# Kernel tuning notes

Measured on AMD Instinct MI355X. Metric: run time of the kernel, lower is better.

Reference implementation:

```python
import jax, jax.numpy as jnp
import numpy as np

N_NODES = 100000
N_EDGES = 1200000
F_IN, F_HID, F_OUT = 128, 64, 40


def gcn_conv(x, W, b, src, dst, n):
    # PyG GCNConv: h = x @ W; add self-loops; symmetric norm; scatter-add; + bias
    h = x @ W  # [N, F]
    loops = jnp.arange(n)
    s = jnp.concatenate([src, loops])
    d = jnp.concatenate([dst, loops])
    deg = jnp.zeros((n,), x.dtype).at[d].add(jnp.asarray(1.0, x.dtype))
    dis = jax.lax.rsqrt(deg)  # deg >= 1 thanks to self-loops
    norm = dis[s] * dis[d]  # [E+N]
    msg = h[s] * norm[:, None]  # gather + scale
    out = jnp.zeros((n, h.shape[1]), x.dtype).at[d].add(msg)  # scatter-add
    return out + b


def setup_inputs() -> dict:
    key = jax.random.key(0)
    ks = jax.random.split(key, 8)
    sc = lambda f: 1.0 / np.sqrt(f)
    return {
        "x": jax.random.normal(ks[0], (N_NODES, F_IN), jnp.float32),
        "edge_index": jax.random.randint(ks[1], (2, N_EDGES), 0, N_NODES, jnp.int64),
        "W1": jax.random.normal(ks[2], (F_IN, F_HID), jnp.float32) * sc(F_IN),
        "b1": jnp.zeros((F_HID,), jnp.float32),
        "W2": jax.random.normal(ks[3], (F_HID, F_HID), jnp.float32) * sc(F_HID),
        "b2": jnp.zeros((F_HID,), jnp.float32),
        "W3": jax.random.normal(ks[4], (F_HID, F_OUT), jnp.float32) * sc(F_HID),
        "b3": jnp.zeros((F_OUT,), jnp.float32),
    }


def reference(x, edge_index, W1, b1, W2, b2, W3, b3):
    src, dst = edge_index[0], edge_index[1]
    n = x.shape[0]
    h = jax.nn.relu(gcn_conv(x, W1, b1, src, dst, n))  # dropout is identity (eval)
    h = jax.nn.relu(gcn_conv(h, W2, b2, src, dst, n))
    out = gcn_conv(h, W3, b3, src, dst, n)
    return jax.nn.log_softmax(out, axis=1)
```

## Files before the change

kernel.cpp:

```cpp
#include <hip/hip_runtime.h>
#include <math.h>


static inline int cdiv(long a, int b) { return (int)((a + b - 1) / b); }

__device__ __forceinline__ unsigned short f2bf(float f) {
    unsigned u = __float_as_uint(f);
    u += 0x7fffu + ((u >> 16) & 1u);
    return (unsigned short)(u >> 16);
}
__device__ __forceinline__ float bf2f(unsigned short b) {
    return __uint_as_float(((unsigned)b) << 16);
}

#define RSH 9
#define RNODES 512
#define GB 256
#define NBMAX 256

__global__ __launch_bounds__(256)
void k_bhist(const int* __restrict__ dst, int* __restrict__ bh,
             int E, int NB, int EPB) {
    __shared__ int bcnt[NBMAX];
    const int tid = threadIdx.x, blk = blockIdx.x;
    for (int i = tid; i < NB; i += 256) bcnt[i] = 0;
    __syncthreads();
    const int e1 = min(E, (blk + 1) * EPB);
    for (int e = blk * EPB + tid; e < e1; e += 256)
        atomicAdd(&bcnt[dst[e] >> RSH], 1);
    __syncthreads();
    for (int i = tid; i < NB; i += 256) bh[i * GB + blk] = bcnt[i];
}

__global__ __launch_bounds__(256)
void k_bscatter(const int* __restrict__ src, const int* __restrict__ dst,
                const int* __restrict__ eoff, int2* __restrict__ ebuf,
                int E, int NB, int EPB) {
    __shared__ int cur[NBMAX];
    const int tid = threadIdx.x, blk = blockIdx.x;
    for (int i = tid; i < NB; i += 256) cur[i] = eoff[i * GB + blk];
    __syncthreads();
    const int e1 = min(E, (blk + 1) * EPB);
    for (int e = blk * EPB + tid; e < e1; e += 256) {
        int d = dst[e];
        int s = src[e];
        int pos = atomicAdd(&cur[d >> RSH], 1);
        ebuf[pos] = make_int2(d, s);
    }
}

__global__ __launch_bounds__(1024)
void k_csr(const int2* __restrict__ ebuf, const int* __restrict__ eoff,
           int* __restrict__ rp, float* __restrict__ dis, int* __restrict__ esrc,
           int N, int E, int NB) {
    __shared__ int cnt[RNODES];
    __shared__ int cur[RNODES];
    __shared__ int sm[1024];
    const int tid = threadIdx.x, b = blockIdx.x;
    const int node0 = b << RSH;
    const int bb = eoff[b * GB];
    const int be = (b + 1 == NB) ? E : eoff[(b + 1) * GB];

    if (tid < RNODES) cnt[tid] = 0;
    __syncthreads();
    for (int e = bb + tid; e < be; e += 1024)
        atomicAdd(&cnt[ebuf[e].x - node0], 1);
    __syncthreads();

    int v = (tid < RNODES) ? cnt[tid] : 0;
    sm[tid] = v;
    __syncthreads();
    for (int off = 1; off < RNODES; off <<= 1) {
        int t = (tid >= off) ? sm[tid - off] : 0;
        __syncthreads();
        sm[tid] += t;
        __syncthreads();
    }
    if (tid < RNODES) {
        int excl = sm[tid] - v;
        cur[tid] = excl;
        int node = node0 + tid;
        if (node < N) {
            rp[node] = bb + excl;
            dis[node] = rsqrtf(1.0f + (float)v);
        }
    }
    if (b == 0 && tid == 0) rp[N] = E;
    __syncthreads();

    for (int e = bb + tid; e < be; e += 1024) {
        int2 ev = ebuf[e];
        int slot = atomicAdd(&cur[ev.x - node0], 1);
        esrc[bb + slot] = ev.y;
    }
}

#define SCAN_B 1024
__global__ void k_scan1(const int* __restrict__ cnt, int* __restrict__ rp,
                        int* __restrict__ bsum, int n) {
    __shared__ int sm[SCAN_B];
    const int tid = threadIdx.x;
    const int gid = blockIdx.x * SCAN_B + tid;
    int v = (gid < n) ? cnt[gid] : 0;
    sm[tid] = v;
    __syncthreads();
    for (int off = 1; off < SCAN_B; off <<= 1) {
        int t = (tid >= off) ? sm[tid - off] : 0;
        __syncthreads();
        sm[tid] += t;
        __syncthreads();
    }
    if (gid < n) rp[gid] = sm[tid] - v;
    if (tid == SCAN_B - 1) bsum[blockIdx.x] = sm[tid];
}

__global__ void k_scan2(int* __restrict__ bsum, int nb) {
    __shared__ int sm[SCAN_B];
    const int tid = threadIdx.x;
    int v = (tid < nb) ? bsum[tid] : 0;
    sm[tid] = v;
    __syncthreads();
    for (int off = 1; off < SCAN_B; off <<= 1) {
        int t = (tid >= off) ? sm[tid - off] : 0;
        __syncthreads();
        sm[tid] += t;
        __syncthreads();
    }
    if (tid < nb) bsum[tid] = sm[tid] - v;
}

__global__ void k_scan3(int* __restrict__ rp, const int* __restrict__ bsum, int n, int E) {
    const int gid = blockIdx.x * SCAN_B + threadIdx.x;
    if (gid < n) rp[gid] += bsum[gid / SCAN_B];
    if (gid == n) rp[n] = E;
}

__device__ __forceinline__ void fma4(float a, const float4& w, float4& acc) {
    acc.x = fmaf(a, w.x, acc.x);
    acc.y = fmaf(a, w.y, acc.y);
    acc.z = fmaf(a, w.z, acc.z);
    acc.w = fmaf(a, w.w, acc.w);
}

template<int K, bool BF16OUT>
__global__ __launch_bounds__(256, 2)
void k_gemm_lds(const float* __restrict__ X, const float* __restrict__ W,
                const float* __restrict__ dis, void* __restrict__ Hout, int N) {
    constexpr int KP = K + 4;
    __shared__ float xs[64 * KP];
    __shared__ float wsh[K * 64];
    const int tid = threadIdx.x;
    const int tx = tid & 15;
    const int ty = tid >> 4;
    const int row0 = blockIdx.x * 64;

    {
        const float4* Wg = (const float4*)W;
        float4* Wl = (float4*)wsh;
#pragma unroll
        for (int i = 0; i < K * 16 / 256; ++i)
            Wl[i * 256 + tid] = Wg[i * 256 + tid];
    }
    {
        constexpr int F4 = K / 4;
        for (int i = tid; i < 64 * F4; i += 256) {
            int r = i / F4, c = i - r * F4;
            int gr = min(row0 + r, N - 1);
            float4 v = *(const float4*)(X + (size_t)gr * K + c * 4);
            *(float4*)(xs + r * KP + c * 4) = v;
        }
    }
    __syncthreads();

    float4 acc0 = {0.f, 0.f, 0.f, 0.f};
    float4 acc1 = {0.f, 0.f, 0.f, 0.f};
    float4 acc2 = {0.f, 0.f, 0.f, 0.f};
    float4 acc3 = {0.f, 0.f, 0.f, 0.f};

    const float* xr0 = xs + (ty * 4 + 0) * KP;
    const float* xr1 = xs + (ty * 4 + 1) * KP;
    const float* xr2 = xs + (ty * 4 + 2) * KP;
    const float* xr3 = xs + (ty * 4 + 3) * KP;

#pragma unroll 2
    for (int k = 0; k < K; k += 4) {
        float4 w0 = *(const float4*)(wsh + (k + 0) * 64 + tx * 4);
        float4 w1 = *(const float4*)(wsh + (k + 1) * 64 + tx * 4);
        float4 w2 = *(const float4*)(wsh + (k + 2) * 64 + tx * 4);
        float4 w3 = *(const float4*)(wsh + (k + 3) * 64 + tx * 4);
        float4 xa = *(const float4*)(xr0 + k);
        float4 xb = *(const float4*)(xr1 + k);
        float4 xc = *(const float4*)(xr2 + k);
        float4 xd = *(const float4*)(xr3 + k);

        fma4(xa.x, w0, acc0); fma4(xa.y, w1, acc0); fma4(xa.z, w2, acc0); fma4(xa.w, w3, acc0);
        fma4(xb.x, w0, acc1); fma4(xb.y, w1, acc1); fma4(xb.z, w2, acc1); fma4(xb.w, w3, acc1);
        fma4(xc.x, w0, acc2); fma4(xc.y, w1, acc2); fma4(xc.z, w2, acc2); fma4(xc.w, w3, acc2);
        fma4(xd.x, w0, acc3); fma4(xd.y, w1, acc3); fma4(xd.z, w2, acc3); fma4(xd.w, w3, acc3);
    }

    const int r = row0 + ty * 4;
#pragma unroll
    for (int i = 0; i < 4; ++i) {
        if (r + i >= N) break;
        float4 a = (i == 0) ? acc0 : (i == 1) ? acc1 : (i == 2) ? acc2 : acc3;
        float d = dis[r + i];
        a.x *= d; a.y *= d; a.z *= d; a.w *= d;
        if (BF16OUT) {
            ushort4 o;
            o.x = f2bf(a.x); o.y = f2bf(a.y); o.z = f2bf(a.z); o.w = f2bf(a.w);
            *(ushort4*)((unsigned short*)Hout + (size_t)(r + i) * 64 + tx * 4) = o;
        } else {
            *(float4*)((float*)Hout + (size_t)(r + i) * 64 + tx * 4) = a;
        }
    }
}

template<int MODE>
__global__ __launch_bounds__(256, 8)
void k_agg(const unsigned short* __restrict__ Hs, const float* __restrict__ dis,
           const int* __restrict__ rp, const int* __restrict__ esrc,
           const float* __restrict__ bias, void* __restrict__ A, int N) {
    const int wave = threadIdx.x >> 6;
    const int lane = threadIdx.x & 63;
    const int node = blockIdx.x * (blockDim.x >> 6) + wave;
    if (node >= N) return;
    const int q  = lane >> 4;
    const int f4 = lane & 15;

    const int e0 = rp[node];
    const int e1 = rp[node + 1];
    float4 acc = {0.f, 0.f, 0.f, 0.f};
    int e = e0 + q;
    for (; e + 4 < e1; e += 8) {
        int s0 = esrc[e];
        int s1 = esrc[e + 4];
        ushort4 h0 = *(const ushort4*)(Hs + (size_t)s0 * 64 + f4 * 4);
        ushort4 h1 = *(const ushort4*)(Hs + (size_t)s1 * 64 + f4 * 4);
        acc.x += bf2f(h0.x) + bf2f(h1.x);
        acc.y += bf2f(h0.y) + bf2f(h1.y);
        acc.z += bf2f(h0.z) + bf2f(h1.z);
        acc.w += bf2f(h0.w) + bf2f(h1.w);
    }
    for (; e < e1; e += 4) {
        int s = esrc[e];
        ushort4 h = *(const ushort4*)(Hs + (size_t)s * 64 + f4 * 4);
        acc.x += bf2f(h.x); acc.y += bf2f(h.y); acc.z += bf2f(h.z); acc.w += bf2f(h.w);
    }
    acc.x += __shfl_xor(acc.x, 16, 64);
    acc.y += __shfl_xor(acc.y, 16, 64);
    acc.z += __shfl_xor(acc.z, 16, 64);
    acc.w += __shfl_xor(acc.w, 16, 64);
    acc.x += __shfl_xor(acc.x, 32, 64);
    acc.y += __shfl_xor(acc.y, 32, 64);
    acc.z += __shfl_xor(acc.z, 32, 64);
    acc.w += __shfl_xor(acc.w, 32, 64);

    if (lane < 16) {
        const float dd = dis[node];
        ushort4 sh = *(const ushort4*)(Hs + (size_t)node * 64 + lane * 4);
        float4 v;
        v.x = (acc.x + bf2f(sh.x)) * dd;
        v.y = (acc.y + bf2f(sh.y)) * dd;
        v.z = (acc.z + bf2f(sh.z)) * dd;
        v.w = (acc.w + bf2f(sh.w)) * dd;
        if (MODE == 0 || MODE == 1) {
            float4 bv = ((const float4*)bias)[lane];
            v.x = fmaxf(v.x + bv.x, 0.f);
            v.y = fmaxf(v.y + bv.y, 0.f);
            v.z = fmaxf(v.z + bv.z, 0.f);
            v.w = fmaxf(v.w + bv.w, 0.f);
        }
        if (MODE == 1) {
            v.x *= dd; v.y *= dd; v.z *= dd; v.w *= dd;
            ushort4 o;
            o.x = f2bf(v.x); o.y = f2bf(v.y); o.z = f2bf(v.z); o.w = f2bf(v.w);
            *(ushort4*)((unsigned short*)A + (size_t)node * 64 + lane * 4) = o;
        } else {
            *(float4*)((float*)A + (size_t)node * 64 + lane * 4) = v;
        }
    }
}

__global__ __launch_bounds__(256, 4)
void k_w3lsm(const float* __restrict__ X, const float* __restrict__ W,
             const float* __restrict__ bias, float* __restrict__ out,
             int N, int npw) {
    const int wid  = blockIdx.x * (blockDim.x >> 6) + (threadIdx.x >> 6);
    const int lane = threadIdx.x & 63;
    const int cl   = (lane < 40) ? lane : 0;

    float w[64];
#pragma unroll
    for (int k = 0; k < 64; ++k) w[k] = W[k * 40 + cl];
    const float bv = bias[cl];

    const int n0 = wid * npw;
    const int n1 = min(n0 + npw, N);
    for (int node = n0; node < n1; ++node) {
        const int un = __builtin_amdgcn_readfirstlane(node);
        const float4* xr = (const float4*)(X + (size_t)un * 64);
        float acc = 0.0f;
#pragma unroll
        for (int j = 0; j < 16; ++j) {
            float4 xv = xr[j];
            acc = fmaf(xv.x, w[4 * j + 0], acc);
            acc = fmaf(xv.y, w[4 * j + 1], acc);
            acc = fmaf(xv.z, w[4 * j + 2], acc);
            acc = fmaf(xv.w, w[4 * j + 3], acc);
        }
        float v = (lane < 40) ? acc + bv : -INFINITY;
        float m = v;
#pragma unroll
        for (int o = 32; o > 0; o >>= 1) m = fmaxf(m, __shfl_xor(m, o, 64));
        float ex = (lane < 40) ? expf(v - m) : 0.0f;
        float s = ex;
#pragma unroll
        for (int o = 32; o > 0; o >>= 1) s += __shfl_xor(s, o, 64);
        if (lane < 40) out[(size_t)node * 40 + lane] = v - m - logf(s);
    }
}

extern "C" void kernel_launch(void* const* d_in, const int* in_sizes, int n_in,
                              void* d_out, int out_size, void* d_ws, size_t ws_size,
                              hipStream_t stream) {
    const float* x  = (const float*)d_in[0];
    const int*   ei = (const int*)d_in[1];
    const float* W1 = (const float*)d_in[2];
    const float* b1 = (const float*)d_in[3];
    const float* W2 = (const float*)d_in[4];
    const float* b2 = (const float*)d_in[5];
    const float* W3 = (const float*)d_in[6];
    const float* b3 = (const float*)d_in[7];
    float* out = (float*)d_out;

    const int N = in_sizes[0] / 128;
    const int E = in_sizes[1] / 2;
    const int* src = ei;
    const int* dst = ei + E;

    const int NB   = cdiv(N, RNODES);
    const int EPB  = cdiv(E, GB);
    const int nscan = NB * GB;

    char* ws = (char*)d_ws;
    char* buf0  = ws;                         ws += (size_t)N * 64 * sizeof(float);
    char* buf1  = ws;                         ws += (size_t)N * 64 * sizeof(float);
    int*   esrc  = (int*)ws;                  ws += (size_t)E * sizeof(int);
    int*   rp    = (int*)ws;                  ws += (size_t)(N + 1) * sizeof(int);
    int*   bsum  = (int*)ws;                  ws += (size_t)SCAN_B * sizeof(int);
    float* dis   = (float*)ws;                ws += (size_t)N * sizeof(float);
    int*   bh    = (int*)ws;                  ws += (size_t)nscan * sizeof(int);
    int*   eoff  = (int*)ws;                  ws += (size_t)(nscan + 1) * sizeof(int);
    int2*  ebuf  = (int2*)buf0;

    const int B = 256;
    const int nbs = cdiv(nscan, SCAN_B);

    k_bhist<<<GB, B, 0, stream>>>(dst, bh, E, NB, EPB);
    k_scan1<<<nbs, SCAN_B, 0, stream>>>(bh, eoff, bsum, nscan);
    k_scan2<<<1, SCAN_B, 0, stream>>>(bsum, nbs);
    k_scan3<<<cdiv(nscan + 1, SCAN_B), SCAN_B, 0, stream>>>(eoff, bsum, nscan, E);
    k_bscatter<<<GB, B, 0, stream>>>(src, dst, eoff, ebuf, E, NB, EPB);
    k_csr<<<NB, 1024, 0, stream>>>(ebuf, eoff, rp, dis, esrc, N, E, NB);

    k_gemm_lds<128, true><<<cdiv(N, 64), B, 0, stream>>>(x, W1, dis, buf0, N);
    k_agg<0><<<cdiv(N, 4), B, 0, stream>>>((const unsigned short*)buf0, dis, rp, esrc, b1, buf1, N);

    k_gemm_lds<64, true><<<cdiv(N, 64), B, 0, stream>>>((const float*)buf1, W2, dis, buf0, N);
    k_agg<1><<<cdiv(N, 4), B, 0, stream>>>((const unsigned short*)buf0, dis, rp, esrc, b2, buf1, N);

    k_agg<2><<<cdiv(N, 4), B, 0, stream>>>((const unsigned short*)buf1, dis, rp, esrc, nullptr, buf0, N);
    const int NW = 4096;
    const int npw = cdiv(N, NW);
    k_w3lsm<<<NW / 4, B, 0, stream>>>((const float*)buf0, W3, b3, out, N, npw);
}
```

Baseline: 336.7 us.

## Reorder layer 3 to transform before aggregating and fuse log_softmax into aggregation

Layer 3 now applies W3 first, producing a 40-wide bf16 Z from the pre-scaled 64-wide layer-2 output, and then aggregates over neighbours. This shrinks per-edge gather traffic from 64 to 40 features. The log_softmax is fused into the new aggregation kernel, which splits each node's edges across six lane groups of ten and reduces them through LDS. The k_agg bias/relu path was also made unconditional, but only modes 0 and 1 are still launched. The trade-off is an extra bf16 rounding of Z and 60 of 64 lanes active during the gather.

```diff
diff --git a/kernel.cpp b/kernel.cpp
--- a/kernel.cpp
+++ b/kernel.cpp
@@ -264,13 +264,11 @@
         v.y = (acc.y + bf2f(sh.y)) * dd;
         v.z = (acc.z + bf2f(sh.z)) * dd;
         v.w = (acc.w + bf2f(sh.w)) * dd;
-        if (MODE == 0 || MODE == 1) {
-            float4 bv = ((const float4*)bias)[lane];
-            v.x = fmaxf(v.x + bv.x, 0.f);
-            v.y = fmaxf(v.y + bv.y, 0.f);
-            v.z = fmaxf(v.z + bv.z, 0.f);
-            v.w = fmaxf(v.w + bv.w, 0.f);
-        }
+        float4 bv = ((const float4*)bias)[lane];
+        v.x = fmaxf(v.x + bv.x, 0.f);
+        v.y = fmaxf(v.y + bv.y, 0.f);
+        v.z = fmaxf(v.z + bv.z, 0.f);
+        v.w = fmaxf(v.w + bv.w, 0.f);
         if (MODE == 1) {
             v.x *= dd; v.y *= dd; v.z *= dd; v.w *= dd;
             ushort4 o;
@@ -283,9 +281,8 @@
 }
 
 __global__ __launch_bounds__(256, 4)
-void k_w3lsm(const float* __restrict__ X, const float* __restrict__ W,
-             const float* __restrict__ bias, float* __restrict__ out,
-             int N, int npw) {
+void k_zgemm(const unsigned short* __restrict__ A2s, const float* __restrict__ W,
+             unsigned short* __restrict__ Z, int N, int npw) {
     const int wid  = blockIdx.x * (blockDim.x >> 6) + (threadIdx.x >> 6);
     const int lane = threadIdx.x & 63;
     const int cl   = (lane < 40) ? lane : 0;
@@ -293,31 +290,94 @@
     float w[64];
 #pragma unroll
     for (int k = 0; k < 64; ++k) w[k] = W[k * 40 + cl];
-    const float bv = bias[cl];
 
     const int n0 = wid * npw;
     const int n1 = min(n0 + npw, N);
     for (int node = n0; node < n1; ++node) {
         const int un = __builtin_amdgcn_readfirstlane(node);
-        const float4* xr = (const float4*)(X + (size_t)un * 64);
+        const uint4* xr = (const uint4*)(A2s + (size_t)un * 64);
         float acc = 0.0f;
 #pragma unroll
-        for (int j = 0; j < 16; ++j) {
-            float4 xv = xr[j];
-            acc = fmaf(xv.x, w[4 * j + 0], acc);
-            acc = fmaf(xv.y, w[4 * j + 1], acc);
-            acc = fmaf(xv.z, w[4 * j + 2], acc);
-            acc = fmaf(xv.w, w[4 * j + 3], acc);
-        }
-        float v = (lane < 40) ? acc + bv : -INFINITY;
-        float m = v;
-#pragma unroll
-        for (int o = 32; o > 0; o >>= 1) m = fmaxf(m, __shfl_xor(m, o, 64));
-        float ex = (lane < 40) ? expf(v - m) : 0.0f;
-        float s = ex;
-#pragma unroll
-        for (int o = 32; o > 0; o >>= 1) s += __shfl_xor(s, o, 64);
-        if (lane < 40) out[(size_t)node * 40 + lane] = v - m - logf(s);
+        for (int j = 0; j < 8; ++j) {
+            uint4 u = xr[j];
+            acc = fmaf(__uint_as_float(u.x << 16),          w[8 * j + 0], acc);
+            acc = fmaf(__uint_as_float(u.x & 0xffff0000u),  w[8 * j + 1], acc);
+            acc = fmaf(__uint_as_float(u.y << 16),          w[8 * j + 2], acc);
+            acc = fmaf(__uint_as_float(u.y & 0xffff0000u),  w[8 * j + 3], acc);
+            acc = fmaf(__uint_as_float(u.z << 16),          w[8 * j + 4], acc);
+            acc = fmaf(__uint_as_float(u.z & 0xffff0000u),  w[8 * j + 5], acc);
+            acc = fmaf(__uint_as_float(u.w << 16),          w[8 * j + 6], acc);
+            acc = fmaf(__uint_as_float(u.w & 0xffff0000u),  w[8 * j + 7], acc);
+        }
+        if (lane < 40) Z[(size_t)node * 40 + lane] = f2bf(acc);
+    }
+}
+
+__global__ __launch_bounds__(256, 8)
+void k_agg40lsm(const unsigned short* __restrict__ Z, const float* __restrict__ dis,
+                const int* __restrict__ rp, const int* __restrict__ esrc,
+                const float* __restrict__ b3, float* __restrict__ out, int N) {
+    __shared__ float4 red[4][64];
+    const int wave = threadIdx.x >> 6;
+    const int lane = threadIdx.x & 63;
+    int node = blockIdx.x * 4 + wave;
+    if (node >= N) node = N - 1;
+    const int q = lane / 10;
+    const int f = lane - q * 10;
+    const bool act = (q < 6);
+
+    const int e0 = rp[node];
+    const int e1 = rp[node + 1];
+    float4 acc = {0.f, 0.f, 0.f, 0.f};
+    if (act) {
+        for (int e = e0 + q; e < e1; e += 6) {
+            int s = esrc[e];
+            ushort4 h = *(const ushort4*)(Z + (size_t)s * 40 + f * 4);
+            acc.x += bf2f(h.x); acc.y += bf2f(h.y); acc.z += bf2f(h.z); acc.w += bf2f(h.w);
+        }
+    }
+    red[wave][lane] = acc;
+    __syncthreads();
+
+    float4 v;
+    float m4 = -INFINITY;
+    if (lane < 10) {
+        float4 a0 = red[wave][lane];
+        float4 a1 = red[wave][10 + lane];
+        float4 a2 = red[wave][20 + lane];
+        float4 a3 = red[wave][30 + lane];
+        float4 a4 = red[wave][40 + lane];
+        float4 a5 = red[wave][50 + lane];
+        v.x = a0.x + a1.x + a2.x + a3.x + a4.x + a5.x;
+        v.y = a0.y + a1.y + a2.y + a3.y + a4.y + a5.y;
+        v.z = a0.z + a1.z + a2.z + a3.z + a4.z + a5.z;
+        v.w = a0.w + a1.w + a2.w + a3.w + a4.w + a5.w;
+        ushort4 sh = *(const ushort4*)(Z + (size_t)node * 40 + lane * 4);
+        const float dd = dis[node];
+        float4 bv = ((const float4*)b3)[lane];
+        v.x = (v.x + bf2f(sh.x)) * dd + bv.x;
+        v.y = (v.y + bf2f(sh.y)) * dd + bv.y;
+        v.z = (v.z + bf2f(sh.z)) * dd + bv.z;
+        v.w = (v.w + bf2f(sh.w)) * dd + bv.w;
+        m4 = fmaxf(fmaxf(v.x, v.y), fmaxf(v.z, v.w));
+    }
+    float m = m4;
+#pragma unroll
+    for (int o = 1; o < 16; o <<= 1) m = fmaxf(m, __shfl_xor(m, o, 64));
+    float es = 0.f;
+    if (lane < 10) {
+        es = expf(v.x - m) + expf(v.y - m) + expf(v.z - m) + expf(v.w - m);
+    }
+#pragma unroll
+    for (int o = 1; o < 16; o <<= 1) es += __shfl_xor(es, o, 64);
+    if (lane < 10) {
+        float ls = logf(es);
+        float4 o4;
+        o4.x = v.x - m - ls;
+        o4.y = v.y - m - ls;
+        o4.z = v.z - m - ls;
+        o4.w = v.w - m - ls;
+        *(float4*)(out + (size_t)node * 40 + lane * 4) = o4;
     }
 }
 
@@ -370,8 +430,10 @@
     k_gemm_lds<64, true><<<cdiv(N, 64), B, 0, stream>>>((const float*)buf1, W2, dis, buf0, N);
     k_agg<1><<<cdiv(N, 4), B, 0, stream>>>((const unsigned short*)buf0, dis, rp, esrc, b2, buf1, N);
 
-    k_agg<2><<<cdiv(N, 4), B, 0, stream>>>((const unsigned short*)buf1, dis, rp, esrc, nullptr, buf0, N);
-    const int NW = 4096;
+    const int NW = 8192;
     const int npw = cdiv(N, NW);
-    k_w3lsm<<<NW / 4, B, 0, stream>>>((const float*)buf0, W3, b3, out, N, npw);
-}
+    k_zgemm<<<NW / 4, B, 0, stream>>>((const unsigned short*)buf1, W3,
+                                      (unsigned short*)buf0, N, npw);
+    k_agg40lsm<<<cdiv(N, 4), B, 0, stream>>>((const unsigned short*)buf0, dis, rp, esrc,
+                                             b3, out, N);
+}
```

New measurement: 343.3 us. Within noise of the previous version (+2.0%).
